# Kernel optimization log

Hardware: AMD Instinct MI355X
Metric: run time of the kernel (lower is better)

Reference implementation:

```python
import jax, jax.numpy as jnp
import numpy as np

N = 50000        # nodes
E = 1600000      # edges (before self loops)
IN = 256         # in_channels
C = 32           # hidden_channels (per head)
H = 4            # heads
OUT = 64         # out_channels
NEG_SLOPE = 0.2  # PyG GATConv default


def setup_inputs() -> dict:
    key = jax.random.key(0)
    ks = jax.random.split(key, 8)
    x = jax.random.normal(ks[0], (N, IN), dtype=jnp.float32)
    edge_index = jax.random.randint(ks[1], (2, E), 0, N, dtype=jnp.int64)
    s = 0.05
    W = jax.random.normal(ks[2], (IN, H * C), dtype=jnp.float32) * s
    att_src = jax.random.normal(ks[3], (H, C), dtype=jnp.float32) * s
    att_dst = jax.random.normal(ks[4], (H, C), dtype=jnp.float32) * s
    bias = jnp.zeros((H * C,), dtype=jnp.float32)
    lin_W = jax.random.normal(ks[5], (H * C, OUT), dtype=jnp.float32) * s
    lin_b = jnp.zeros((OUT,), dtype=jnp.float32)
    return {"x": x, "edge_index": edge_index, "W": W, "att_src": att_src,
            "att_dst": att_dst, "bias": bias, "lin_W": lin_W, "lin_b": lin_b}


def reference(x, edge_index, W, att_src, att_dst, bias, lin_W, lin_b):
    # Linear transform per head: [N, H, C]
    h = (x @ W).reshape(N, H, C)
    # Per-node attention halves (PyG GATConv): [N, H]
    a_src = jnp.einsum('nhc,hc->nh', h, att_src)
    a_dst = jnp.einsum('nhc,hc->nh', h, att_dst)
    # Add self loops (PyG default add_self_loops=True)
    loop = jnp.arange(N, dtype=edge_index.dtype)
    src = jnp.concatenate([edge_index[0], loop])  # message source j
    dst = jnp.concatenate([edge_index[1], loop])  # message target i
    # Edge attention logits: LeakyReLU(a_src[j] + a_dst[i])  -> [E+N, H]
    e = jax.nn.leaky_relu(a_src[src] + a_dst[dst], negative_slope=NEG_SLOPE)
    # Segment softmax over incoming edges of each destination node
    emax = jax.lax.stop_gradient(jax.ops.segment_max(e, dst, num_segments=N))
    emax = jnp.where(jnp.isfinite(emax), emax, 0.0)
    ex = jnp.exp(e - emax[dst])
    denom = jax.ops.segment_sum(ex, dst, num_segments=N)
    alpha = ex / denom[dst]  # [E+N, H]; self loops guarantee denom > 0
    # Weighted scatter-sum of source features: [N, H, C]
    msg = alpha[:, :, None] * h[src]
    agg = jax.ops.segment_sum(msg, dst, num_segments=N)
    out = agg.reshape(N, H * C) + bias  # concat heads + bias
    out = jax.nn.elu(out)
    return out @ lin_W + lin_b
```

## Files before the change

### kernel.cpp

```cpp
#include <hip/hip_runtime.h>
#include <cstdint>
#include <cstddef>

#define N_NODES 50000
#define N_EDGES 1600000
#define TOT_E   (N_EDGES + N_NODES)
#define IN_DIM  256
#define HC      128
#define NHEAD   4
#define OUT_DIM 64

#define SHIFT   7
#define BSZ     128
#define NBUK    ((N_NODES + BSZ - 1) / BSZ)
#define CHUNK   2048
#define EPT     8
#define NCHUNK  ((TOT_E + CHUNK - 1) / CHUNK)
#define CAP     6144
#define QCAP    1792

#define XPAD 264
#define HPAD 132
#define K1_NB ((N_NODES + 63) / 64)

typedef __attribute__((ext_vector_type(8))) short bf16x8;
typedef __attribute__((ext_vector_type(4))) float f32x4;

static __device__ __forceinline__ uint16_t f2bf(float f) {
    uint32_t u = __float_as_uint(f);
    uint32_t r = (u + 0x7fffu + ((u >> 16) & 1u)) >> 16;
    return (uint16_t)r;
}
static __device__ __forceinline__ float bf_lo(uint32_t u) {
    return __uint_as_float(u << 16);
}
static __device__ __forceinline__ float bf_hi(uint32_t u) {
    return __uint_as_float(u & 0xffff0000u);
}

__global__ __launch_bounds__(256) void w2bf(const float* __restrict__ W,
                                            uint16_t* __restrict__ wt,
                                            int* __restrict__ gcur) {
    int idx = blockIdx.x * 256 + threadIdx.x;
    int n = idx >> 8, k = idx & 255;
    wt[idx] = f2bf(W[(size_t)k * HC + n]);
    if (idx < NBUK) gcur[idx] = 0;
}

__global__ __launch_bounds__(256) void k1p3(const float* __restrict__ x,
                                            const uint16_t* __restrict__ wt,
                                            const float* __restrict__ att_src,
                                            const float* __restrict__ att_dst,
                                            uint16_t* __restrict__ hb,
                                            float* __restrict__ a_src,
                                            float* __restrict__ a_dst,
                                            const int* __restrict__ ei,
                                            int* __restrict__ gcur,
                                            uint32_t* __restrict__ binned) {
    __shared__ char smem[64 * 528];
    __shared__ float att_s[HC], att_d[HC];
    const int tid = threadIdx.x;

    if (blockIdx.x < K1_NB) {
        uint16_t* xs = (uint16_t*)smem;
        float*    hs = (float*)smem;
        const int wave = tid >> 6;
        const int lane = tid & 63;
        const int m    = lane & 15;
        const int q    = lane >> 4;
        const int row0 = blockIdx.x * 64;

        if (tid < HC) { att_s[tid] = att_src[tid]; att_d[tid] = att_dst[tid]; }

        for (int i = tid * 4; i < 64 * IN_DIM; i += 1024) {
            int r = i >> 8, c = i & 255;
            int gr = row0 + r;
            float4 v = make_float4(0.f, 0.f, 0.f, 0.f);
            if (gr < N_NODES) v = *(const float4*)(x + (size_t)gr * IN_DIM + c);
            uint32_t lo = (uint32_t)f2bf(v.x) | ((uint32_t)f2bf(v.y) << 16);
            uint32_t hi = (uint32_t)f2bf(v.z) | ((uint32_t)f2bf(v.w) << 16);
            *(uint2*)(xs + r * XPAD + c) = make_uint2(lo, hi);
        }
        __syncthreads();

        f32x4 acc[8];
        #pragma unroll
        for (int t = 0; t < 8; ++t) acc[t] = (f32x4){0.f, 0.f, 0.f, 0.f};

        const int arow = wave * 16 + m;
        #pragma unroll
        for (int ks = 0; ks < IN_DIM; ks += 32) {
            bf16x8 a = *(const bf16x8*)(xs + arow * XPAD + ks + q * 8);
            #pragma unroll
            for (int t = 0; t < 8; ++t) {
                bf16x8 b = *(const bf16x8*)(wt + (size_t)(t * 16 + m) * IN_DIM + ks + q * 8);
                acc[t] = __builtin_amdgcn_mfma_f32_16x16x32_bf16(a, b, acc[t], 0, 0, 0);
            }
        }
        __syncthreads();

        #pragma unroll
        for (int t = 0; t < 8; ++t)
            #pragma unroll
            for (int r = 0; r < 4; ++r)
                hs[(wave * 16 + q * 4 + r) * HPAD + t * 16 + m] = acc[t][r];
        __syncthreads();

        for (int i = tid * 4; i < 64 * HC; i += 1024) {
            int r = i >> 7, c = i & 127;
            if (row0 + r < N_NODES) {
                float4 v = *(const float4*)(hs + r * HPAD + c);
                uint32_t lo = (uint32_t)f2bf(v.x) | ((uint32_t)f2bf(v.y) << 16);
                uint32_t hi = (uint32_t)f2bf(v.z) | ((uint32_t)f2bf(v.w) << 16);
                *(uint2*)(hb + (size_t)(row0 + r) * HC + c) = make_uint2(lo, hi);
            }
        }
        {
            int r = tid >> 2, hd = tid & 3;
            if (row0 + r < N_NODES) {
                float s = 0.f, d = 0.f;
                #pragma unroll
                for (int j = 0; j < 32; ++j) {
                    float v = hs[r * HPAD + hd * 32 + j];
                    s = fmaf(v, att_s[hd * 32 + j], s);
                    d = fmaf(v, att_d[hd * 32 + j], d);
                }
                a_src[(row0 + r) * NHEAD + hd] = s;
                a_dst[(row0 + r) * NHEAD + hd] = d;
            }
        }
    } else {
        int* hist = (int*)smem;
        int* lcur = hist + NBUK;
        for (int i = tid; i < NBUK; i += 256) hist[i] = 0;
        __syncthreads();

        uint32_t wreg[EPT];
        const int base = (blockIdx.x - K1_NB) * CHUNK;
        #pragma unroll
        for (int k = 0; k < EPT; ++k) {
            int e = base + k * 256 + tid;
            uint32_t word = 0xFFFFFFFFu;
            if (e < TOT_E) {
                int src, dst;
                if (e < N_EDGES) { src = ei[e]; dst = ei[N_EDGES + e]; }
                else             { src = e - N_EDGES; dst = src; }
                int b = dst >> SHIFT;
                word = (uint32_t)src | ((uint32_t)(dst & (BSZ - 1)) << 16)
                     | ((uint32_t)b << 23);
                atomicAdd(&hist[b], 1);
            }
            wreg[k] = word;
        }
        __syncthreads();
        for (int i = tid; i < NBUK; i += 256) {
            int c = hist[i];
            lcur[i] = c ? atomicAdd(&gcur[i], c) : 0;
        }
        __syncthreads();
        #pragma unroll
        for (int k = 0; k < EPT; ++k) {
            uint32_t word = wreg[k];
            if (word != 0xFFFFFFFFu) {
                int b = (int)(word >> 23);
                int pos = atomicAdd(&lcur[b], 1);
                if (pos < CAP) binned[(size_t)b * CAP + pos] = word;
            }
        }
    }
}

__global__ __launch_bounds__(256) void q4_agg(const uint32_t* __restrict__ binned,
                                              const int* __restrict__ gcur,
                                              const uint32_t* __restrict__ hb32,
                                              const float* __restrict__ a_src,
                                              const float* __restrict__ a_dst,
                                              const float* __restrict__ bias,
                                              uint32_t* __restrict__ actb) {
    __shared__ uint32_t ewb[QCAP];
    __shared__ uint32_t ew2[QCAP];
    __shared__ int ncnt[32], nbeg[32], ncur[32];
    __shared__ int tot;
    const int b   = blockIdx.x >> 2;
    const int sub = blockIdx.x & 3;
    const int tid = threadIdx.x;

    int cnt = gcur[b];
    if (cnt > CAP) cnt = CAP;
    if (tid == 0) tot = 0;
    if (tid < 32) ncnt[tid] = 0;
    __syncthreads();

    const uint32_t* bb = binned + (size_t)b * CAP;
    for (int i = tid; i < cnt; i += 256) {
        uint32_t word = bb[i];
        int dl = (word >> 16) & 127;
        if ((dl >> 5) == sub) {
            int pos = atomicAdd(&tot, 1);
            if (pos < QCAP) ewb[pos] = word;
            atomicAdd(&ncnt[dl & 31], 1);
        }
    }
    __syncthreads();
    int T = tot;
    if (T > QCAP) T = QCAP;

    if (tid < 32) {
        int v = ncnt[tid];
        int inc = v;
        #pragma unroll
        for (int d = 1; d < 32; d <<= 1) {
            int t = __shfl_up(inc, d, 64);
            if (tid >= d) inc += t;
        }
        nbeg[tid] = inc - v;
        ncur[tid] = inc - v;
    }
    __syncthreads();
    for (int i = tid; i < T; i += 256) {
        uint32_t word = ewb[i];
        int ln  = (word >> 16) & 31;
        int pos = atomicAdd(&ncur[ln], 1);
        ew2[pos] = word & 0xFFFFu;
    }
    __syncthreads();

    const int wave = tid >> 6;
    const int lane = tid & 63;
    const int head = lane >> 4;
    const uint32_t* hbl = hb32 + lane;
    const float*    ash = a_src + head;

    for (int k = 0; k < 8; ++k) {
        const int ln   = wave * 8 + k;
        const int node = b * BSZ + sub * 32 + ln;
        if (node >= N_NODES) continue;

        const float ad = a_dst[node * NHEAD + head];
        int p = nbeg[ln];
        const int end = p + ncnt[ln];

        float l = 0.f, acc0 = 0.f, acc1 = 0.f;

        for (; p + 4 <= end; p += 4) {
            int s0 = (int)ew2[p + 0];
            int s1 = (int)ew2[p + 1];
            int s2 = (int)ew2[p + 2];
            int s3 = (int)ew2[p + 3];
            float e0 = ash[s0 * NHEAD] + ad;
            float e1 = ash[s1 * NHEAD] + ad;
            float e2 = ash[s2 * NHEAD] + ad;
            float e3 = ash[s3 * NHEAD] + ad;
            uint32_t u0 = hbl[(size_t)s0 * 64];
            uint32_t u1 = hbl[(size_t)s1 * 64];
            uint32_t u2 = hbl[(size_t)s2 * 64];
            uint32_t u3 = hbl[(size_t)s3 * 64];
            e0 = fmaxf(e0, 0.2f * e0);
            e1 = fmaxf(e1, 0.2f * e1);
            e2 = fmaxf(e2, 0.2f * e2);
            e3 = fmaxf(e3, 0.2f * e3);
            float w0 = __expf(e0), w1 = __expf(e1);
            float w2 = __expf(e2), w3 = __expf(e3);
            l += (w0 + w1) + (w2 + w3);
            acc0 = fmaf(w0, bf_lo(u0), acc0);
            acc1 = fmaf(w0, bf_hi(u0), acc1);
            acc0 = fmaf(w1, bf_lo(u1), acc0);
            acc1 = fmaf(w1, bf_hi(u1), acc1);
            acc0 = fmaf(w2, bf_lo(u2), acc0);
            acc1 = fmaf(w2, bf_hi(u2), acc1);
            acc0 = fmaf(w3, bf_lo(u3), acc0);
            acc1 = fmaf(w3, bf_hi(u3), acc1);
        }
        for (; p < end; ++p) {
            int s = (int)ew2[p];
            float e = ash[s * NHEAD] + ad;
            e = fmaxf(e, 0.2f * e);
            float w = __expf(e);
            uint32_t u = hbl[(size_t)s * 64];
            l += w;
            acc0 = fmaf(w, bf_lo(u), acc0);
            acc1 = fmaf(w, bf_hi(u), acc1);
        }

        const int c0 = lane << 1;
        float inv = 1.f / l;
        float o0 = acc0 * inv + bias[c0];
        float o1 = acc1 * inv + bias[c0 + 1];
        o0 = (o0 > 0.f) ? o0 : (__expf(o0) - 1.f);
        o1 = (o1 > 0.f) ? o1 : (__expf(o1) - 1.f);
        actb[(size_t)node * 64 + lane] = (uint32_t)f2bf(o0) | ((uint32_t)f2bf(o1) << 16);
    }
}

__global__ __launch_bounds__(512) void k7_out(const uint32_t* __restrict__ actb,
                                              const float* __restrict__ linW,
                                              const float* __restrict__ linb,
                                              float* __restrict__ out) {
    __shared__ float sW[HC * OUT_DIM];
    __shared__ float srow[32 * HC];
    const int tid   = threadIdx.x;
    const int node0 = blockIdx.x * 32;

    for (int i = tid * 4; i < HC * OUT_DIM; i += 512 * 4)
        *(float4*)(sW + i) = *(const float4*)(linW + i);
    {
        int i = tid * 4;
        int r = i >> 6, cw = i & 63;
        int node = node0 + r;
        uint4 v = make_uint4(0, 0, 0, 0);
        if (node < N_NODES) v = *(const uint4*)(actb + (size_t)node * 64 + cw);
        float* d = srow + r * HC + cw * 2;
        d[0] = bf_lo(v.x); d[1] = bf_hi(v.x);
        d[2] = bf_lo(v.y); d[3] = bf_hi(v.y);
        d[4] = bf_lo(v.z); d[5] = bf_hi(v.z);
        d[6] = bf_lo(v.w); d[7] = bf_hi(v.w);
    }
    __syncthreads();

    const int r    = tid >> 4;
    const int colb = (tid & 15) << 2;
    float4 acc = *(const float4*)(linb + colb);
    const float* rp = srow + r * HC;

    #pragma unroll
    for (int k = 0; k < HC; k += 4) {
        float4 xv = *(const float4*)(rp + k);
        float4 w0 = *(const float4*)(sW + (k + 0) * OUT_DIM + colb);
        float4 w1 = *(const float4*)(sW + (k + 1) * OUT_DIM + colb);
        float4 w2 = *(const float4*)(sW + (k + 2) * OUT_DIM + colb);
        float4 w3 = *(const float4*)(sW + (k + 3) * OUT_DIM + colb);
        acc.x += xv.x * w0.x; acc.x += xv.y * w1.x; acc.x += xv.z * w2.x; acc.x += xv.w * w3.x;
        acc.y += xv.x * w0.y; acc.y += xv.y * w1.y; acc.y += xv.z * w2.y; acc.y += xv.w * w3.y;
        acc.z += xv.x * w0.z; acc.z += xv.y * w1.z; acc.z += xv.z * w2.z; acc.z += xv.w * w3.z;
        acc.w += xv.x * w0.w; acc.w += xv.y * w1.w; acc.w += xv.z * w2.w; acc.w += xv.w * w3.w;
    }

    int node = node0 + r;
    if (node < N_NODES)
        *(float4*)(out + (size_t)node * OUT_DIM + colb) = acc;
}

extern "C" void kernel_launch(void* const* d_in, const int* in_sizes, int n_in,
                              void* d_out, int out_size, void* d_ws, size_t ws_size,
                              hipStream_t stream) {
    (void)in_sizes; (void)n_in; (void)out_size; (void)ws_size;
    const float* x       = (const float*)d_in[0];
    const int*   ei      = (const int*)d_in[1];
    const float* W       = (const float*)d_in[2];
    const float* att_src = (const float*)d_in[3];
    const float* att_dst = (const float*)d_in[4];
    const float* bias    = (const float*)d_in[5];
    const float* linW    = (const float*)d_in[6];
    const float* linb    = (const float*)d_in[7];
    float*       out     = (float*)d_out;

    char*  ws  = (char*)d_ws;
    size_t off = 0;
    auto alloc = [&](size_t bytes) -> void* {
        void* p = ws + off;
        off += (bytes + 255) & ~(size_t)255;
        return p;
    };
    uint16_t* hb     = (uint16_t*)alloc((size_t)N_NODES * HC * 2);
    uint16_t* wt     = (uint16_t*)alloc((size_t)HC * IN_DIM * 2);
    uint32_t* actb   = (uint32_t*)alloc((size_t)N_NODES * 64 * 4);
    float*    a_src  = (float*)alloc((size_t)N_NODES * NHEAD * 4);
    float*    a_dst  = (float*)alloc((size_t)N_NODES * NHEAD * 4);
    int*      gcur   = (int*)alloc((size_t)NBUK * 4);
    uint32_t* binned = (uint32_t*)alloc((size_t)NBUK * CAP * 4);

    w2bf<<<(HC * IN_DIM) / 256, 256, 0, stream>>>(W, wt, gcur);
    k1p3<<<K1_NB + NCHUNK, 256, 0, stream>>>(x, wt, att_src, att_dst,
                                             hb, a_src, a_dst,
                                             ei, gcur, binned);
    q4_agg<<<NBUK * 4, 256, 0, stream>>>(binned, gcur, (const uint32_t*)hb,
                                         a_src, a_dst, bias, actb);
    k7_out<<<(N_NODES + 31) / 32, 512, 0, stream>>>(actb, linW, linb, out);
}
```

Measured before the change: 244.5 us.

## Bin edges directly into 32-node buckets and drop per-sub-block refiltering

Edges are now binned into 1563 buckets of 32 destination nodes, not 128-node buckets that four aggregation blocks each rescanned and filtered. Each binning chunk grows to 16384 edges and reads the edge list twice (a histogram pass, then a scatter pass) instead of holding words in registers. The aggregation kernel uses 512 threads per bucket with per-wave histograms and a 16-bit local edge list. This removes the 4x redundant reads of bucket contents, at the cost of rereading edge_index and more global atomics on many small buckets. Buckets above 1792 entries are still truncated.

```diff
diff --git a/kernel.cpp b/kernel.cpp
--- a/kernel.cpp
+++ b/kernel.cpp
@@ -10,14 +10,12 @@
 #define NHEAD   4
 #define OUT_DIM 64
 
-#define SHIFT   7
-#define BSZ     128
-#define NBUK    ((N_NODES + BSZ - 1) / BSZ)
-#define CHUNK   2048
-#define EPT     8
+#define BSHIFT  5
+#define BNODES  32
+#define NBUK    ((N_NODES + BNODES - 1) / BNODES)
+#define QCAP    1792
+#define CHUNK   16384
 #define NCHUNK  ((TOT_E + CHUNK - 1) / CHUNK)
-#define CAP     6144
-#define QCAP    1792
 
 #define XPAD 264
 #define HPAD 132
@@ -135,22 +133,12 @@
         for (int i = tid; i < NBUK; i += 256) hist[i] = 0;
         __syncthreads();
 
-        uint32_t wreg[EPT];
-        const int base = (blockIdx.x - K1_NB) * CHUNK;
-        #pragma unroll
-        for (int k = 0; k < EPT; ++k) {
-            int e = base + k * 256 + tid;
-            uint32_t word = 0xFFFFFFFFu;
-            if (e < TOT_E) {
-                int src, dst;
-                if (e < N_EDGES) { src = ei[e]; dst = ei[N_EDGES + e]; }
-                else             { src = e - N_EDGES; dst = src; }
-                int b = dst >> SHIFT;
-                word = (uint32_t)src | ((uint32_t)(dst & (BSZ - 1)) << 16)
-                     | ((uint32_t)b << 23);
-                atomicAdd(&hist[b], 1);
-            }
-            wreg[k] = word;
+        const int e0 = (blockIdx.x - K1_NB) * CHUNK;
+        int e1 = e0 + CHUNK; if (e1 > TOT_E) e1 = TOT_E;
+
+        for (int e = e0 + tid; e < e1; e += 256) {
+            int dst = (e < N_EDGES) ? ei[N_EDGES + e] : (e - N_EDGES);
+            atomicAdd(&hist[dst >> BSHIFT], 1);
         }
         __syncthreads();
         for (int i = tid; i < NBUK; i += 256) {
@@ -158,55 +146,52 @@
             lcur[i] = c ? atomicAdd(&gcur[i], c) : 0;
         }
         __syncthreads();
-        #pragma unroll
-        for (int k = 0; k < EPT; ++k) {
-            uint32_t word = wreg[k];
-            if (word != 0xFFFFFFFFu) {
-                int b = (int)(word >> 23);
-                int pos = atomicAdd(&lcur[b], 1);
-                if (pos < CAP) binned[(size_t)b * CAP + pos] = word;
-            }
-        }
-    }
-}
-
-__global__ __launch_bounds__(256) void q4_agg(const uint32_t* __restrict__ binned,
+        for (int e = e0 + tid; e < e1; e += 256) {
+            int src, dst;
+            if (e < N_EDGES) { src = ei[e]; dst = ei[N_EDGES + e]; }
+            else             { src = e - N_EDGES; dst = src; }
+            int b = dst >> BSHIFT;
+            int pos = atomicAdd(&lcur[b], 1);
+            if (pos < QCAP)
+                binned[(size_t)b * QCAP + pos] =
+                    (uint32_t)src | ((uint32_t)(dst & (BNODES - 1)) << 16);
+        }
+    }
+}
+
+__global__ __launch_bounds__(512) void q4_agg(const uint32_t* __restrict__ binned,
                                               const int* __restrict__ gcur,
                                               const uint32_t* __restrict__ hb32,
                                               const float* __restrict__ a_src,
                                               const float* __restrict__ a_dst,
                                               const float* __restrict__ bias,
                                               uint32_t* __restrict__ actb) {
-    __shared__ uint32_t ewb[QCAP];
-    __shared__ uint32_t ew2[QCAP];
-    __shared__ int ncnt[32], nbeg[32], ncur[32];
-    __shared__ int tot;
-    const int b   = blockIdx.x >> 2;
-    const int sub = blockIdx.x & 3;
+    __shared__ uint32_t ew[QCAP];
+    __shared__ uint16_t ew2[QCAP];
+    __shared__ int ncnt[8][32];
+    __shared__ int nbeg[32], ncur[32], ntot[32];
+    const int b   = blockIdx.x;
     const int tid = threadIdx.x;
+    const int wv  = tid >> 6;
 
     int cnt = gcur[b];
-    if (cnt > CAP) cnt = CAP;
-    if (tid == 0) tot = 0;
-    if (tid < 32) ncnt[tid] = 0;
-    __syncthreads();
-
-    const uint32_t* bb = binned + (size_t)b * CAP;
-    for (int i = tid; i < cnt; i += 256) {
-        uint32_t word = bb[i];
-        int dl = (word >> 16) & 127;
-        if ((dl >> 5) == sub) {
-            int pos = atomicAdd(&tot, 1);
-            if (pos < QCAP) ewb[pos] = word;
-            atomicAdd(&ncnt[dl & 31], 1);
-        }
-    }
-    __syncthreads();
-    int T = tot;
-    if (T > QCAP) T = QCAP;
+    if (cnt > QCAP) cnt = QCAP;
+
+    if (tid < 256) { ((int*)ncnt)[tid] = 0; }
+    __syncthreads();
+
+    const uint32_t* bb = binned + (size_t)b * QCAP;
+    for (int i = tid; i < cnt; i += 512) {
+        uint32_t w = bb[i];
+        ew[i] = w;
+        atomicAdd(&ncnt[wv][(w >> 16) & 31], 1);
+    }
+    __syncthreads();
 
     if (tid < 32) {
-        int v = ncnt[tid];
+        int v = 0;
+        #pragma unroll
+        for (int w = 0; w < 8; ++w) v += ncnt[w][tid];
         int inc = v;
         #pragma unroll
         for (int d = 1; d < 32; d <<= 1) {
@@ -215,30 +200,30 @@
         }
         nbeg[tid] = inc - v;
         ncur[tid] = inc - v;
-    }
-    __syncthreads();
-    for (int i = tid; i < T; i += 256) {
-        uint32_t word = ewb[i];
-        int ln  = (word >> 16) & 31;
+        ntot[tid] = v;
+    }
+    __syncthreads();
+    for (int i = tid; i < cnt; i += 512) {
+        uint32_t w = ew[i];
+        int ln  = (w >> 16) & 31;
         int pos = atomicAdd(&ncur[ln], 1);
-        ew2[pos] = word & 0xFFFFu;
-    }
-    __syncthreads();
-
-    const int wave = tid >> 6;
+        ew2[pos] = (uint16_t)w;
+    }
+    __syncthreads();
+
     const int lane = tid & 63;
     const int head = lane >> 4;
     const uint32_t* hbl = hb32 + lane;
     const float*    ash = a_src + head;
 
-    for (int k = 0; k < 8; ++k) {
-        const int ln   = wave * 8 + k;
-        const int node = b * BSZ + sub * 32 + ln;
+    for (int k = 0; k < 4; ++k) {
+        const int ln   = wv * 4 + k;
+        const int node = b * BNODES + ln;
         if (node >= N_NODES) continue;
 
         const float ad = a_dst[node * NHEAD + head];
         int p = nbeg[ln];
-        const int end = p + ncnt[ln];
+        const int end = p + ntot[ln];
 
         float l = 0.f, acc0 = 0.f, acc1 = 0.f;
 
@@ -367,13 +352,13 @@
     float*    a_src  = (float*)alloc((size_t)N_NODES * NHEAD * 4);
     float*    a_dst  = (float*)alloc((size_t)N_NODES * NHEAD * 4);
     int*      gcur   = (int*)alloc((size_t)NBUK * 4);
-    uint32_t* binned = (uint32_t*)alloc((size_t)NBUK * CAP * 4);
+    uint32_t* binned = (uint32_t*)alloc((size_t)NBUK * QCAP * 4);
 
     w2bf<<<(HC * IN_DIM) / 256, 256, 0, stream>>>(W, wt, gcur);
     k1p3<<<K1_NB + NCHUNK, 256, 0, stream>>>(x, wt, att_src, att_dst,
                                              hb, a_src, a_dst,
                                              ei, gcur, binned);
-    q4_agg<<<NBUK * 4, 256, 0, stream>>>(binned, gcur, (const uint32_t*)hb,
-                                         a_src, a_dst, bias, actb);
+    q4_agg<<<NBUK, 512, 0, stream>>>(binned, gcur, (const uint32_t*)hb,
+                                     a_src, a_dst, bias, actb);
     k7_out<<<(N_NODES + 31) / 32, 512, 0, stream>>>(actb, linW, linb, out);
 }
```

After: 267.6 us. 9.4% more time.
